# Kernel tuning notes

Hardware: AMD Instinct MI355X
Metric: run time of the kernel (lower is better)

## Reference

```python
import jax, jax.numpy as jnp
import numpy as np

N = 10000          # nodes
E_RAND = 320000    # random edges (avg degree 32)
F_IN = 512         # nfeat
HID = 256          # args.hid
HEADS = 8          # args.head
FH = HID // HEADS  # 32 per head
NCLASS = 40
TAU = 0.5
LAMDA = 0.5
K = 2


def setup_inputs() -> dict:
    key = jax.random.key(0)
    ks = jax.random.split(key, 16)
    # edge list: random edges + self-loops (so every dst segment is non-empty)
    src = jnp.concatenate([jax.random.randint(ks[0], (E_RAND,), 0, N), jnp.arange(N)])
    dst = jnp.concatenate([jax.random.randint(ks[1], (E_RAND,), 0, N), jnp.arange(N)])
    s = 0.05  # small init scale keeps exp() in attention/bind_loss stable
    return {
        "x": jax.random.normal(ks[2], (N, F_IN), jnp.float32),
        "src": src, "dst": dst,
        "W0": jax.random.normal(ks[3], (F_IN, HEADS, FH), jnp.float32) * s,
        "a0s": jax.random.normal(ks[4], (HEADS, FH), jnp.float32) * s,
        "a0d": jax.random.normal(ks[5], (HEADS, FH), jnp.float32) * s,
        "W1": jax.random.normal(ks[6], (HID, HEADS, FH), jnp.float32) * s,
        "a1s": jax.random.normal(ks[7], (HEADS, FH), jnp.float32) * s,
        "a1d": jax.random.normal(ks[8], (HEADS, FH), jnp.float32) * s,
        "W2": jax.random.normal(ks[9], (HID, HEADS, FH), jnp.float32) * s,
        "a2s": jax.random.normal(ks[10], (HEADS, FH), jnp.float32) * s,
        "a2d": jax.random.normal(ks[11], (HEADS, FH), jnp.float32) * s,
        "Wout": jax.random.normal(ks[12], (HID, HEADS, NCLASS), jnp.float32) * s,
        "aos": jax.random.normal(ks[13], (HEADS, NCLASS), jnp.float32) * s,
        "aod": jax.random.normal(ks[14], (HEADS, NCLASS), jnp.float32) * s,
    }


def _gat_layer(x, W, a_s, a_d, src, dst):
    """Sparse multi-head GAT layer: gather -> edge softmax -> scatter."""
    n = x.shape[0]
    h = jnp.einsum('nf,fhd->nhd', x, W)              # [N,H,Fh]
    es = jnp.sum(h * a_s, axis=-1)                    # [N,H]
    ed = jnp.sum(h * a_d, axis=-1)                    # [N,H]
    e = jax.nn.leaky_relu(es[src] + ed[dst], 0.2)     # [E,H]
    m = jax.ops.segment_max(e, dst, num_segments=n)   # per-dst max (stable softmax)
    w = jnp.exp(e - m[dst])
    z = jax.ops.segment_sum(w, dst, num_segments=n)
    alpha = w / z[dst]                                # [E,H]
    return jax.ops.segment_sum(alpha[:, :, None] * h[src], dst, num_segments=n)  # [N,H,Fh]


def _bind_loss(z):
    # z1 == z2 == z in the original call site: refl_sim == between_sim
    zn = z / jnp.maximum(jnp.linalg.norm(z, axis=1, keepdims=True), 1e-12)
    S = jnp.exp(jnp.matmul(zn, zn.T) / TAU)           # [N,N]
    d = jnp.diagonal(S)
    off = jnp.sum(S, axis=1) - d                      # masked (off-diagonal) row sum
    CT = -jnp.log(d / (off + off))                    # neg_c2.sum + neg_c3.sum
    return jnp.mean(CT)


def reference(x, src, dst, W0, a0s, a0d, W1, a1s, a1d, W2, a2s, a2d, Wout, aos, aod):
    layers = [(W0, a0s, a0d), (W1, a1s, a1d), (W2, a2s, a2d)]
    last = x
    loss = jnp.float32(0.0)
    for i, (W, as_, ad_) in enumerate(layers):
        cur = jax.nn.elu(_gat_layer(last, W, as_, ad_, src, dst))
        cur = cur.reshape(cur.shape[0], -1)           # concat heads -> [N, HID]
        if i > 0:
            beta = LAMDA / (i + 2)                    # MaskLayer(last, cur, lamda, i+2)
            cur = beta * last + (1.0 - beta) * cur
            if i % K == 0:
                loss = loss + _bind_loss(cur)
        last = cur
    out = _gat_layer(last, Wout, aos, aod, src, dst).mean(axis=1)  # avg heads -> [N,C]
    return (jax.nn.log_softmax(out, axis=1), loss)
```

## Files before the change

kernel.cpp:

```cpp
#include <hip/hip_runtime.h>
#include <hip/hip_bf16.h>
#include <math.h>

#define NN_F_IN   512
#define NN_HID    256
#define NN_HEADS  8
#define NN_FH     32
#define NN_NCLASS 40
#define TAU_F     0.5f
#define LAMDA_F   0.5f
#define ZN_SCALE  1.6986436f

typedef __attribute__((ext_vector_type(8))) short bf16x8;
typedef __attribute__((ext_vector_type(4))) float f32x4;

static __device__ __forceinline__ float lrelu02(float x) { return x >= 0.f ? x : 0.2f * x; }
static __device__ __forceinline__ float elu1(float x)    { return x > 0.f ? x : expm1f(x); }
static __device__ __forceinline__ float b2f(unsigned short u) {
    unsigned int x = ((unsigned int)u) << 16;
    return __uint_as_float(x);
}
static __device__ __forceinline__ unsigned short f2b(float f) {
    __hip_bfloat16 hb = __float2bfloat16(f);
    return *reinterpret_cast<unsigned short*>(&hb);
}

__global__ void prep_kernel(const float* __restrict__ x,
                            const float* __restrict__ W0, const float* __restrict__ W1,
                            const float* __restrict__ W2, const float* __restrict__ Wo,
                            unsigned short* __restrict__ Xb,
                            unsigned short* __restrict__ Wt0, unsigned short* __restrict__ Wt1,
                            unsigned short* __restrict__ Wt2, unsigned short* __restrict__ Wto,
                            int n4X) {
    int i = blockIdx.x * 256 + threadIdx.x;
    if (i < n4X) {
        float4 v = *(const float4*)(x + (size_t)i * 4);
        ushort4 o;
        o.x = f2b(v.x); o.y = f2b(v.y); o.z = f2b(v.z); o.w = f2b(v.w);
        *(ushort4*)(Xb + (size_t)i * 4) = o;
        return;
    }
    i -= n4X;
    if (i < 256 * 512) {
        int np = i >> 9, k = i & 511;
        Wt0[i] = f2b(W0[(size_t)k * 256 + np]);
        return;
    }
    i -= 256 * 512;
    if (i < 256 * 256) {
        int np = i >> 8, k = i & 255;
        Wt1[i] = f2b(W1[(size_t)k * 256 + np]);
        return;
    }
    i -= 256 * 256;
    if (i < 256 * 256) {
        int np = i >> 8, k = i & 255;
        Wt2[i] = f2b(W2[(size_t)k * 256 + np]);
        return;
    }
    i -= 256 * 256;
    if (i < 384 * 256) {
        int np = i >> 8, k = i & 255;
        Wto[i] = f2b(np < 320 ? Wo[(size_t)k * 320 + np] : 0.f);
    }
}

__global__ __launch_bounds__(256) void fc_attn_mfma(
    const unsigned short* __restrict__ A, const unsigned short* __restrict__ B,
    unsigned short* __restrict__ H, const float* __restrict__ As_,
    const float* __restrict__ Ad_, float* __restrict__ es, float* __restrict__ ed,
    int M, int K) {
    const int ldH = 256;
    int t = threadIdx.x, lane = t & 63, wid = t >> 6;
    int wrow = wid >> 1, wcol = wid & 1;
    int l15 = lane & 15, lg = lane >> 4;
    int mbase = blockIdx.y * 64 + wrow * 32;
    int nbase = blockIdx.x * 64 + wcol * 32;

    const unsigned short* Ap[2];
    const unsigned short* Bp[2];
#pragma unroll
    for (int m = 0; m < 2; ++m) {
        int rr = mbase + m * 16 + l15;
        if (rr > M - 1) rr = M - 1;
        Ap[m] = A + (size_t)rr * K + lg * 8;
        Bp[m] = B + (size_t)(nbase + m * 16 + l15) * K + lg * 8;
    }
    f32x4 acc[2][2];
#pragma unroll
    for (int m = 0; m < 2; ++m)
#pragma unroll
        for (int nn = 0; nn < 2; ++nn)
#pragma unroll
            for (int r = 0; r < 4; ++r) acc[m][nn][r] = 0.f;

    bf16x8 aP[2], bP[2], aQ[2], bQ[2];
#pragma unroll
    for (int m = 0; m < 2; ++m) {
        aP[m] = *(const bf16x8*)(Ap[m]);
        bP[m] = *(const bf16x8*)(Bp[m]);
    }
    int nhalf = K >> 6;
    int kk = 32;
    for (int it = 0; it < nhalf; ++it) {
#pragma unroll
        for (int m = 0; m < 2; ++m) {
            aQ[m] = *(const bf16x8*)(Ap[m] + kk);
            bQ[m] = *(const bf16x8*)(Bp[m] + kk);
        }
#pragma unroll
        for (int m = 0; m < 2; ++m)
#pragma unroll
            for (int nn = 0; nn < 2; ++nn)
                acc[m][nn] = __builtin_amdgcn_mfma_f32_16x16x32_bf16(aP[m], bP[nn], acc[m][nn], 0, 0, 0);
        if (it + 1 < nhalf) {
#pragma unroll
            for (int m = 0; m < 2; ++m) {
                aP[m] = *(const bf16x8*)(Ap[m] + kk + 32);
                bP[m] = *(const bf16x8*)(Bp[m] + kk + 32);
            }
        }
#pragma unroll
        for (int m = 0; m < 2; ++m)
#pragma unroll
            for (int nn = 0; nn < 2; ++nn)
                acc[m][nn] = __builtin_amdgcn_mfma_f32_16x16x32_bf16(aQ[m], bQ[nn], acc[m][nn], 0, 0, 0);
        kk += 64;
    }
#pragma unroll
    for (int m = 0; m < 2; ++m) {
#pragma unroll
        for (int nn = 0; nn < 2; ++nn) {
            int col = nbase + nn * 16 + l15;
#pragma unroll
            for (int r = 0; r < 4; ++r) {
                int row = mbase + m * 16 + lg * 4 + r;
                if (row < M) H[(size_t)row * ldH + col] = f2b(acc[m][nn][r]);
            }
        }
    }
    int hh = blockIdx.x * 2 + wcol;
    float a0 = As_[hh * 32 + l15], a1 = As_[hh * 32 + 16 + l15];
    float d0 = Ad_[hh * 32 + l15], d1 = Ad_[hh * 32 + 16 + l15];
#pragma unroll
    for (int m = 0; m < 2; ++m) {
#pragma unroll
        for (int r = 0; r < 4; ++r) {
            float ps = acc[m][0][r] * a0 + acc[m][1][r] * a1;
            float pd = acc[m][0][r] * d0 + acc[m][1][r] * d1;
            ps += __shfl_xor(ps, 1, 64); pd += __shfl_xor(pd, 1, 64);
            ps += __shfl_xor(ps, 2, 64); pd += __shfl_xor(pd, 2, 64);
            ps += __shfl_xor(ps, 4, 64); pd += __shfl_xor(pd, 4, 64);
            ps += __shfl_xor(ps, 8, 64); pd += __shfl_xor(pd, 8, 64);
            if (l15 == 0) {
                int row = mbase + m * 16 + lg * 4 + r;
                if (row < M) {
                    es[row * NN_HEADS + hh] = ps;
                    ed[row * NN_HEADS + hh] = pd;
                }
            }
        }
    }
}

__global__ __launch_bounds__(256) void fc_mfma(const unsigned short* __restrict__ A,
                                               const unsigned short* __restrict__ B,
                                               unsigned short* __restrict__ H,
                                               int M, int K, int ncols, int ldH) {
    int t = threadIdx.x, lane = t & 63, wid = t >> 6;
    int wrow = wid >> 1, wcol = wid & 1;
    int l15 = lane & 15, lg = lane >> 4;
    int mbase = blockIdx.y * 64 + wrow * 32;
    int nbase = blockIdx.x * 64 + wcol * 32;

    const unsigned short* Ap[2];
    const unsigned short* Bp[2];
#pragma unroll
    for (int m = 0; m < 2; ++m) {
        int rr = mbase + m * 16 + l15;
        if (rr > M - 1) rr = M - 1;
        Ap[m] = A + (size_t)rr * K + lg * 8;
        Bp[m] = B + (size_t)(nbase + m * 16 + l15) * K + lg * 8;
    }
    f32x4 acc[2][2];
#pragma unroll
    for (int m = 0; m < 2; ++m)
#pragma unroll
        for (int nn = 0; nn < 2; ++nn)
#pragma unroll
            for (int r = 0; r < 4; ++r) acc[m][nn][r] = 0.f;

    bf16x8 aP[2], bP[2], aQ[2], bQ[2];
#pragma unroll
    for (int m = 0; m < 2; ++m) {
        aP[m] = *(const bf16x8*)(Ap[m]);
        bP[m] = *(const bf16x8*)(Bp[m]);
    }
    int nhalf = K >> 6;
    int kk = 32;
    for (int it = 0; it < nhalf; ++it) {
#pragma unroll
        for (int m = 0; m < 2; ++m) {
            aQ[m] = *(const bf16x8*)(Ap[m] + kk);
            bQ[m] = *(const bf16x8*)(Bp[m] + kk);
        }
#pragma unroll
        for (int m = 0; m < 2; ++m)
#pragma unroll
            for (int nn = 0; nn < 2; ++nn)
                acc[m][nn] = __builtin_amdgcn_mfma_f32_16x16x32_bf16(aP[m], bP[nn], acc[m][nn], 0, 0, 0);
        if (it + 1 < nhalf) {
#pragma unroll
            for (int m = 0; m < 2; ++m) {
                aP[m] = *(const bf16x8*)(Ap[m] + kk + 32);
                bP[m] = *(const bf16x8*)(Bp[m] + kk + 32);
            }
        }
#pragma unroll
        for (int m = 0; m < 2; ++m)
#pragma unroll
            for (int nn = 0; nn < 2; ++nn)
                acc[m][nn] = __builtin_amdgcn_mfma_f32_16x16x32_bf16(aQ[m], bQ[nn], acc[m][nn], 0, 0, 0);
        kk += 64;
    }
#pragma unroll
    for (int m = 0; m < 2; ++m) {
#pragma unroll
        for (int nn = 0; nn < 2; ++nn) {
            int col = nbase + nn * 16 + l15;
            if (col >= ncols) continue;
#pragma unroll
            for (int r = 0; r < 4; ++r) {
                int row = mbase + m * 16 + lg * 4 + r;
                if (row < M) H[(size_t)row * ldH + col] = f2b(acc[m][nn][r]);
            }
        }
    }
}

__global__ void attn_kernel(const unsigned short* __restrict__ Hm, const float* __restrict__ As,
                            const float* __restrict__ Ad, float* __restrict__ es,
                            float* __restrict__ ed, int n, int df) {
    int idx = blockIdx.x * blockDim.x + threadIdx.x;
    if (idx >= n * NN_HEADS) return;
    int nn = idx / NN_HEADS, hh = idx - nn * NN_HEADS;
    const unsigned short* hp = Hm + (size_t)nn * NN_HEADS * df + hh * df;
    const float* ap = As + hh * df;
    const float* bp = Ad + hh * df;
    float s1 = 0.f, s2 = 0.f;
    for (int d = 0; d < df; d += 4) {
        ushort4 hv = *(const ushort4*)(hp + d);
        float4 av = *(const float4*)(ap + d);
        float4 bv = *(const float4*)(bp + d);
        float h0 = b2f(hv.x), h1 = b2f(hv.y), h2 = b2f(hv.z), h3 = b2f(hv.w);
        s1 += h0 * av.x + h1 * av.y + h2 * av.z + h3 * av.w;
        s2 += h0 * bv.x + h1 * bv.y + h2 * bv.z + h3 * bv.w;
    }
    es[idx] = s1;
    ed[idx] = s2;
}

__global__ __launch_bounds__(256) void edge_wz(
    const float* __restrict__ es, const float* __restrict__ ed,
    const int* __restrict__ csr_src, const int* __restrict__ row_start,
    float* __restrict__ wC, float* __restrict__ zinv, int n) {
    int lane = threadIdx.x & 63;
    int nn   = blockIdx.x * 4 + (threadIdx.x >> 6);
    if (nn >= n) return;
    int s0 = row_start[nn], s1 = row_start[nn + 1];
    int h    = lane & 7;
    int slot = lane >> 3;
    float edh = ed[nn * NN_HEADS + h];
    float z = 0.f;
    for (int e = s0 + slot; e < s1; e += 8) {
        int sv = csr_src[e];
        float w = __expf(lrelu02(es[sv * NN_HEADS + h] + edh));
        wC[(size_t)e * NN_HEADS + h] = w;
        z += w;
    }
    z += __shfl_xor(z, 8, 64);
    z += __shfl_xor(z, 16, 64);
    z += __shfl_xor(z, 32, 64);
    if (slot == 0) zinv[nn * NN_HEADS + h] = 1.f / z;
}

__global__ void count_kernel(const int* __restrict__ dst, int* __restrict__ counts, int E) {
    int e = blockIdx.x * blockDim.x + threadIdx.x;
    if (e < E) atomicAdd(&counts[dst[e]], 1);
}

__global__ void scan_kernel(const int* __restrict__ counts, int* __restrict__ row_start,
                            int* __restrict__ cursor, int n) {
    __shared__ int s[1024];
    int t  = threadIdx.x;
    int ch = (n + 1023) / 1024;
    int lo = t * ch;
    int sum = 0;
    for (int j = 0; j < ch; ++j) {
        int i = lo + j;
        if (i < n) sum += counts[i];
    }
    s[t] = sum;
    __syncthreads();
    for (int off = 1; off < 1024; off <<= 1) {
        int v = 0;
        if (t >= off) v = s[t - off];
        __syncthreads();
        s[t] += v;
        __syncthreads();
    }
    int run = (t == 0) ? 0 : s[t - 1];
    for (int j = 0; j < ch; ++j) {
        int i = lo + j;
        if (i < n) {
            row_start[i] = run;
            cursor[i] = run;
            run += counts[i];
        }
    }
    if (t == 1023) row_start[n] = s[1023];
}

__global__ void scatter_kernel(const int* __restrict__ src, const int* __restrict__ dst,
                               int* __restrict__ cursor, int* __restrict__ csr_src, int E) {
    int e = blockIdx.x * blockDim.x + threadIdx.x;
    if (e < E) {
        int d   = dst[e];
        int pos = atomicAdd(&cursor[d], 1);
        csr_src[pos] = src[e];
    }
}

__global__ __launch_bounds__(256) void gather_hidden(
    const unsigned short* __restrict__ Hm, const float* __restrict__ es,
    const float* __restrict__ ed, const int* __restrict__ csr_src,
    const int* __restrict__ row_start, const unsigned short* __restrict__ last,
    unsigned short* __restrict__ out, int n, float beta,
    unsigned short* __restrict__ znb, float* __restrict__ dvec) {
    int lane = threadIdx.x & 63;
    int nn   = blockIdx.x * 4 + (threadIdx.x >> 6);
    if (nn >= n) return;
    int s0 = row_start[nn], s1 = row_start[nn + 1];
    int h2 = lane >> 3;
    float edh = ed[nn * NN_HEADS + h2];

    float zacc = 0.f;
    float a0 = 0.f, a1 = 0.f, a2 = 0.f, a3 = 0.f;
    int fullEnd = s0 + ((s1 - s0) & ~15);
    int e = s0;
    for (; e < fullEnd; e += 16) {
        int idx[16];
        float q[16];
#pragma unroll
        for (int j = 0; j < 16; ++j) idx[j] = csr_src[e + j];
#pragma unroll
        for (int j = 0; j < 16; ++j) q[j] = es[idx[j] * NN_HEADS + h2];
        ushort4 r[16];
#pragma unroll
        for (int j = 0; j < 16; ++j) r[j] = *(const ushort4*)&Hm[(size_t)idx[j] * NN_HID + lane * 4];
#pragma unroll
        for (int j = 0; j < 16; ++j) {
            float w = __expf(lrelu02(q[j] + edh));
            zacc += w;
            a0 += w * b2f(r[j].x); a1 += w * b2f(r[j].y);
            a2 += w * b2f(r[j].z); a3 += w * b2f(r[j].w);
        }
    }
    if (e < s1) {
        int c = s1 - e;
        int idx[16];
        float q[16];
#pragma unroll
        for (int j = 0; j < 16; ++j) idx[j] = csr_src[(j < c) ? e + j : e];
#pragma unroll
        for (int j = 0; j < 16; ++j) q[j] = es[idx[j] * NN_HEADS + h2];
        ushort4 r[16];
#pragma unroll
        for (int j = 0; j < 16; ++j) r[j] = *(const ushort4*)&Hm[(size_t)idx[j] * NN_HID + lane * 4];
#pragma unroll
        for (int j = 0; j < 16; ++j) {
            if (j < c) {
                float w = __expf(lrelu02(q[j] + edh));
                zacc += w;
                a0 += w * b2f(r[j].x); a1 += w * b2f(r[j].y);
                a2 += w * b2f(r[j].z); a3 += w * b2f(r[j].w);
            }
        }
    }
    float zi = 1.f / zacc;
    float v0 = elu1(a0 * zi), v1 = elu1(a1 * zi), v2 = elu1(a2 * zi), v3 = elu1(a3 * zi);
    if (beta >= 0.f) {
        ushort4 lv = *(const ushort4*)&last[(size_t)nn * NN_HID + lane * 4];
        v0 = beta * b2f(lv.x) + (1.f - beta) * v0;
        v1 = beta * b2f(lv.y) + (1.f - beta) * v1;
        v2 = beta * b2f(lv.z) + (1.f - beta) * v2;
        v3 = beta * b2f(lv.w) + (1.f - beta) * v3;
    }
    ushort4 o;
    o.x = f2b(v0); o.y = f2b(v1); o.z = f2b(v2); o.w = f2b(v3);
    *(ushort4*)&out[(size_t)nn * NN_HID + lane * 4] = o;

    if (znb) {
        float ss = v0 * v0 + v1 * v1 + v2 * v2 + v3 * v3;
        ss += __shfl_xor(ss, 1, 64);
        ss += __shfl_xor(ss, 2, 64);
        ss += __shfl_xor(ss, 4, 64);
        ss += __shfl_xor(ss, 8, 64);
        ss += __shfl_xor(ss, 16, 64);
        ss += __shfl_xor(ss, 32, 64);
        float m = fmaxf(sqrtf(ss), 1e-12f);
        float sc = ZN_SCALE / m;
        ushort4 zo;
        zo.x = f2b(v0 * sc); zo.y = f2b(v1 * sc);
        zo.z = f2b(v2 * sc); zo.w = f2b(v3 * sc);
        *(ushort4*)&znb[(size_t)nn * NN_HID + lane * 4] = zo;
        if (lane == 0) dvec[nn] = __expf((ss / (m * m)) * (1.f / TAU_F));
    }
}

__global__ void gather_final(const unsigned short* __restrict__ Hm, const float* __restrict__ wC,
                             const float* __restrict__ zinv, const int* __restrict__ csr_src,
                             const int* __restrict__ row_start, float* __restrict__ dout, int n) {
    int nn = blockIdx.x;
    __shared__ float accs[NN_HEADS * NN_NCLASS];
    int t = threadIdx.x;
    int s0 = row_start[nn], s1 = row_start[nn + 1];
    int hh = t / NN_NCLASS;
    float acc = 0.f;
    const int LD = NN_HEADS * NN_NCLASS;
    int fullEnd = s0 + ((s1 - s0) & ~15);
    int e = s0;
    for (; e < fullEnd; e += 16) {
        int idx[16];
        float wv[16];
#pragma unroll
        for (int j = 0; j < 16; ++j) {
            idx[j] = csr_src[e + j];
            wv[j]  = wC[(size_t)(e + j) * NN_HEADS + hh];
        }
        float v[16];
#pragma unroll
        for (int j = 0; j < 16; ++j) v[j] = b2f(Hm[(size_t)idx[j] * LD + t]);
#pragma unroll
        for (int j = 0; j < 16; ++j) acc += wv[j] * v[j];
    }
    if (e < s1) {
        int c = s1 - e;
        int idx[16];
        float wv[16];
#pragma unroll
        for (int j = 0; j < 16; ++j) {
            int p = (j < c) ? e + j : e;
            idx[j] = csr_src[p];
            wv[j]  = wC[(size_t)p * NN_HEADS + hh];
        }
        float v[16];
#pragma unroll
        for (int j = 0; j < 16; ++j) v[j] = b2f(Hm[(size_t)idx[j] * LD + t]);
#pragma unroll
        for (int j = 0; j < 16; ++j) {
            if (j < c) acc += wv[j] * v[j];
        }
    }
    accs[t] = acc * zinv[nn * NN_HEADS + hh];
    __syncthreads();
    if (t < 64) {
        float v = -INFINITY;
        if (t < NN_NCLASS) {
            float sacc = 0.f;
#pragma unroll
            for (int h2 = 0; h2 < NN_HEADS; ++h2) sacc += accs[h2 * NN_NCLASS + t];
            v = sacc * (1.f / NN_HEADS);
        }
        float mx = v;
#pragma unroll
        for (int o = 1; o < 64; o <<= 1) mx = fmaxf(mx, __shfl_xor(mx, o, 64));
        float ex = (t < NN_NCLASS) ? expf(v - mx) : 0.f;
        float se = ex;
#pragma unroll
        for (int o = 1; o < 64; o <<= 1) se += __shfl_xor(se, o, 64);
        if (t < NN_NCLASS) dout[(size_t)nn * NN_NCLASS + t] = (v - mx) - logf(se);
    }
}

__global__ __launch_bounds__(256) void gram_mfma(const short* __restrict__ znb,
                                                 float* __restrict__ P2d, int n,
                                                 int T, int nwg, int Npad) {
    __shared__ short As[2][128 * 64];
    __shared__ short Bs[2][128 * 64];

    int b = blockIdx.x;
    int q = nwg >> 3, r8 = nwg & 7, xc = b & 7, oo = b >> 3;
    int sid = (xc < r8 ? xc * (q + 1) : r8 * (q + 1) + (xc - r8) * q) + oo;
    int bi = 0, rem = sid;
    while (rem >= T - bi) { rem -= T - bi; ++bi; }
    int bj = bi + rem;
    int i0 = bi * 128, j0 = bj * 128;

    int t    = threadIdx.x;
    int lane = t & 63;
    int wid  = t >> 6;
    int wrow = wid >> 1, wcol = wid & 1;
    int l15  = lane & 15, lg = lane >> 4;
    int srow = lane >> 3;
    int sch  = lane & 7;

    f32x4 acc[4][4];
#pragma unroll
    for (int m = 0; m < 4; ++m)
#pragma unroll
        for (int nn = 0; nn < 4; ++nn)
#pragma unroll
            for (int r = 0; r < 4; ++r) acc[m][nn][r] = 0.f;

    bf16x8 sa[2][4], sb[2][4];
#pragma unroll
    for (int sl = 0; sl < 2; ++sl)
#pragma unroll
        for (int s = 0; s < 4; ++s) {
            int row = wid * 32 + s * 8 + srow;
            int gch = sch ^ (row & 7);
            sa[sl][s] = *(const bf16x8*)(znb + (size_t)(i0 + row) * NN_HID + sl * 64 + gch * 8);
            sb[sl][s] = *(const bf16x8*)(znb + (size_t)(j0 + row) * NN_HID + sl * 64 + gch * 8);
        }

#pragma unroll
    for (int kt = 0; kt < 2; ++kt) {
#pragma unroll
        for (int sl = 0; sl < 2; ++sl)
#pragma unroll
            for (int s = 0; s < 4; ++s) {
                int row = wid * 32 + s * 8 + srow;
                *(bf16x8*)(&As[sl][row * 64 + sch * 8]) = sa[sl][s];
                *(bf16x8*)(&Bs[sl][row * 64 + sch * 8]) = sb[sl][s];
            }
        __syncthreads();
        if (kt == 0) {
#pragma unroll
            for (int sl = 0; sl < 2; ++sl)
#pragma unroll
                for (int s = 0; s < 4; ++s) {
                    int row = wid * 32 + s * 8 + srow;
                    int gch = sch ^ (row & 7);
                    sa[sl][s] = *(const bf16x8*)(znb + (size_t)(i0 + row) * NN_HID + 128 + sl * 64 + gch * 8);
                    sb[sl][s] = *(const bf16x8*)(znb + (size_t)(j0 + row) * NN_HID + 128 + sl * 64 + gch * 8);
                }
        }
#pragma unroll
        for (int sl = 0; sl < 2; ++sl) {
#pragma unroll
            for (int ks = 0; ks < 2; ++ks) {
                bf16x8 av[4], bv[4];
#pragma unroll
                for (int m = 0; m < 4; ++m) {
                    int Ra = wrow * 64 + m * 16 + l15;
                    int Rb = wcol * 64 + m * 16 + l15;
                    int ca = (ks * 4 + lg) ^ (Ra & 7);
                    int cb = (ks * 4 + lg) ^ (Rb & 7);
                    av[m] = *(const bf16x8*)(&As[sl][Ra * 64 + ca * 8]);
                    bv[m] = *(const bf16x8*)(&Bs[sl][Rb * 64 + cb * 8]);
                }
#pragma unroll
                for (int m = 0; m < 4; ++m)
#pragma unroll
                    for (int nn = 0; nn < 4; ++nn)
                        acc[m][nn] = __builtin_amdgcn_mfma_f32_16x16x32_bf16(av[m], bv[nn], acc[m][nn], 0, 0, 0);
            }
        }
        if (kt == 0) __syncthreads();
    }

    int i0w = i0 + wrow * 64;
    int j0w = j0 + wcol * 64;
    bool diag = (bj == bi);
    if (bj == T - 1) {
#pragma unroll
        for (int m = 0; m < 4; ++m)
#pragma unroll
            for (int nn = 0; nn < 4; ++nn) {
                int gj = j0w + nn * 16 + l15;
                bool jok = gj < n;
#pragma unroll
                for (int r = 0; r < 4; ++r) {
                    int gi = i0w + m * 16 + lg * 4 + r;
                    acc[m][nn][r] = (jok && gi < n) ? __builtin_exp2f(acc[m][nn][r]) : 0.f;
                }
            }
    } else {
#pragma unroll
        for (int m = 0; m < 4; ++m)
#pragma unroll
            for (int nn = 0; nn < 4; ++nn)
#pragma unroll
                for (int r = 0; r < 4; ++r)
                    acc[m][nn][r] = __builtin_exp2f(acc[m][nn][r]);
    }
    float* rowslot = P2d + (size_t)(2 * bj + wcol) * Npad;
#pragma unroll
    for (int m = 0; m < 4; ++m) {
#pragma unroll
        for (int r = 0; r < 4; ++r) {
            float v = acc[m][0][r] + acc[m][1][r] + acc[m][2][r] + acc[m][3][r];
            v += __shfl_xor(v, 1, 64);
            v += __shfl_xor(v, 2, 64);
            v += __shfl_xor(v, 4, 64);
            v += __shfl_xor(v, 8, 64);
            if (l15 == 0) {
                int gi = i0w + m * 16 + lg * 4 + r;
                if (gi < n) rowslot[gi] = v;
            }
        }
    }
    if (!diag) {
        float* colslot = P2d + (size_t)(2 * bi + wrow) * Npad;
#pragma unroll
        for (int nn = 0; nn < 4; ++nn) {
            float v = 0.f;
#pragma unroll
            for (int m = 0; m < 4; ++m)
#pragma unroll
                for (int r = 0; r < 4; ++r) v += acc[m][nn][r];
            v += __shfl_xor(v, 16, 64);
            v += __shfl_xor(v, 32, 64);
            if (lg == 0) {
                int gj = j0w + nn * 16 + l15;
                if (gj < n) colslot[gj] = v;
            }
        }
    }
}

__global__ void fold_kernel(const float* __restrict__ P2d, float* __restrict__ R,
                            int n, int slots, int Npad) {
    int i = blockIdx.x * 256 + threadIdx.x;
    if (i >= n) return;
    const float* p = P2d + i;
    float s0 = 0.f, s1 = 0.f, s2 = 0.f, s3 = 0.f;
    int sl = 0;
    for (; sl + 4 <= slots; sl += 4) {
        s0 += p[(size_t)(sl + 0) * Npad];
        s1 += p[(size_t)(sl + 1) * Npad];
        s2 += p[(size_t)(sl + 2) * Npad];
        s3 += p[(size_t)(sl + 3) * Npad];
    }
    for (; sl < slots; ++sl) s0 += p[(size_t)sl * Npad];
    R[i] = (s0 + s1) + (s2 + s3);
}

__global__ void loss_kernel(const float* __restrict__ R, const float* __restrict__ dvec,
                            float* __restrict__ out_loss, int n) {
    __shared__ float s[1024];
    int t = threadIdx.x;
    float sum = 0.f;
    for (int i = t; i < n; i += 1024) {
        float d   = dvec[i];
        float off = R[i] - d;
        sum += -logf(d / (off + off));
    }
    s[t] = sum;
    __syncthreads();
    for (int o = 512; o > 0; o >>= 1) {
        if (t < o) s[t] += s[t + o];
        __syncthreads();
    }
    if (t == 0) *out_loss = s[0] / n;
}

extern "C" void kernel_launch(void* const* d_in, const int* in_sizes, int n_in,
                              void* d_out, int out_size, void* d_ws, size_t ws_size,
                              hipStream_t stream) {
    const float* x   = (const float*)d_in[0];
    const int*   src = (const int*)d_in[1];
    const int*   dst = (const int*)d_in[2];
    const float* W0  = (const float*)d_in[3];
    const float* a0s = (const float*)d_in[4];
    const float* a0d = (const float*)d_in[5];
    const float* W1  = (const float*)d_in[6];
    const float* a1s = (const float*)d_in[7];
    const float* a1d = (const float*)d_in[8];
    const float* W2  = (const float*)d_in[9];
    const float* a2s = (const float*)d_in[10];
    const float* a2d = (const float*)d_in[11];
    const float* Wout= (const float*)d_in[12];
    const float* aos = (const float*)d_in[13];
    const float* aod = (const float*)d_in[14];

    int N = in_sizes[0] / NN_F_IN;
    int E = in_sizes[1];
    int Npad = ((N + 127) / 128) * 128;
    int T = Npad / 128;
    int nwg = T * (T + 1) / 2;
    float* out = (float*)d_out;

    char*  ws  = (char*)d_ws;
    size_t off = 0;
    auto alloc = [&](size_t bytes) -> void* {
        void* p = ws + off;
        off += bytes;
        off = (off + 255) & ~(size_t)255;
        return p;
    };
    unsigned short* Hb = (unsigned short*)alloc((size_t)N * 320 * 2);
    unsigned short* znb = (unsigned short*)alloc((size_t)Npad * NN_HID * 2);
    unsigned short* Bl = (unsigned short*)alloc((size_t)N * NN_HID * 2);
    unsigned short* Bc = (unsigned short*)alloc((size_t)N * NN_HID * 2);
    size_t xbBytes = (size_t)N * NN_F_IN * 2;
    size_t p2Bytes = (size_t)2 * T * Npad * 4;
    void* XbP2d = alloc(xbBytes > p2Bytes ? xbBytes : p2Bytes);
    unsigned short* Xb  = (unsigned short*)XbP2d;
    float*          P2d = (float*)XbP2d;
    unsigned short* Wt0 = (unsigned short*)alloc((size_t)256 * 512 * 2);
    unsigned short* Wt1 = (unsigned short*)alloc((size_t)256 * 256 * 2);
    unsigned short* Wt2 = (unsigned short*)alloc((size_t)256 * 256 * 2);
    unsigned short* Wto = (unsigned short*)alloc((size_t)384 * 256 * 2);
    float* es     = (float*)alloc((size_t)N * NN_HEADS * 4);
    float* ed     = (float*)alloc((size_t)N * NN_HEADS * 4);
    float* wC     = (float*)alloc((size_t)E * NN_HEADS * 4);
    float* zinvA  = (float*)alloc((size_t)N * NN_HEADS * 4);
    float* Rrow   = (float*)alloc((size_t)N * 4);
    float* dvec   = (float*)alloc((size_t)N * 4);
    int*   counts = (int*)alloc((size_t)N * 4);
    int*   rs     = (int*)alloc((size_t)(N + 1) * 4);
    int*   cursor = (int*)alloc((size_t)N * 4);
    int*   csr    = (int*)alloc((size_t)E * 4);

    hipMemsetAsync(counts, 0, (size_t)N * 4, stream);
    if (Npad > N)
        hipMemsetAsync(znb + (size_t)N * NN_HID, 0, (size_t)(Npad - N) * NN_HID * 2, stream);
    count_kernel<<<(E + 255) / 256, 256, 0, stream>>>(dst, counts, E);
    scan_kernel<<<1, 1024, 0, stream>>>(counts, rs, cursor, N);
    scatter_kernel<<<(E + 255) / 256, 256, 0, stream>>>(src, dst, cursor, csr, E);

    int n4X = N * NN_F_IN / 4;
    int prepTotal = n4X + 256 * 512 + 256 * 256 + 256 * 256 + 384 * 256;
    prep_kernel<<<(prepTotal + 255) / 256, 256, 0, stream>>>(
        x, W0, W1, W2, Wout, Xb, Wt0, Wt1, Wt2, Wto, n4X);

    int atGrid = (N * NN_HEADS + 255) / 256;
    int ghGrid = (N + 3) / 4;
    int mT64 = (N + 63) / 64;

    fc_attn_mfma<<<dim3(4, mT64), 256, 0, stream>>>(Xb, Wt0, Hb, a0s, a0d, es, ed, N, 512);
    gather_hidden<<<ghGrid, 256, 0, stream>>>(Hb, es, ed, csr, rs, nullptr, Bl, N, -1.f,
                                              nullptr, nullptr);

    fc_attn_mfma<<<dim3(4, mT64), 256, 0, stream>>>(Bl, Wt1, Hb, a1s, a1d, es, ed, N, 256);
    gather_hidden<<<ghGrid, 256, 0, stream>>>(Hb, es, ed, csr, rs, Bl, Bc, N, LAMDA_F / 3.f,
                                              nullptr, nullptr);

    fc_attn_mfma<<<dim3(4, mT64), 256, 0, stream>>>(Bc, Wt2, Hb, a2s, a2d, es, ed, N, 256);
    gather_hidden<<<ghGrid, 256, 0, stream>>>(Hb, es, ed, csr, rs, Bc, Bl, N, LAMDA_F / 4.f,
                                              znb, dvec);

    gram_mfma<<<nwg, 256, 0, stream>>>((const short*)znb, P2d, N, T, nwg, Npad);
    fold_kernel<<<(N + 255) / 256, 256, 0, stream>>>(P2d, Rrow, N, 2 * T, Npad);
    loss_kernel<<<1, 1024, 0, stream>>>(Rrow, dvec, out + (size_t)N * NN_NCLASS, N);

    fc_mfma<<<dim3(5, mT64), 256, 0, stream>>>(Bl, Wto, Hb, N, 256, 320, 320);
    attn_kernel<<<atGrid, 256, 0, stream>>>(Hb, aos, aod, es, ed, N, NN_NCLASS);
    edge_wz<<<ghGrid, 256, 0, stream>>>(es, ed, csr, rs, wC, zinvA, N);
    gather_final<<<N, NN_HEADS * NN_NCLASS, 0, stream>>>(Hb, wC, zinvA, csr, rs, out, N);
}
```

Measured before the change: 375.5 us.

## Merge output FC GEMM into gram kernel launch and halve gather unroll

The output-layer FC GEMM is folded into the gram kernel as extra leading blocks. The FC tiles then run alongside the gram tiles in one launch instead of after them, and the attention and edge-weight kernels are moved ahead of the fold and loss kernels. Separately, the gather loops in gather_hidden and gather_final are unrolled by 8 instead of 16, trading memory-level parallelism for lower register pressure and a smaller tail. The FC blocks now share the gram kernel's large LDS allocation even though they don't use it, which may cap co-residency for those blocks.

```diff
diff --git a/kernel.cpp b/kernel.cpp
--- a/kernel.cpp
+++ b/kernel.cpp
@@ -158,81 +158,6 @@
                     es[row * NN_HEADS + hh] = ps;
                     ed[row * NN_HEADS + hh] = pd;
                 }
-            }
-        }
-    }
-}
-
-__global__ __launch_bounds__(256) void fc_mfma(const unsigned short* __restrict__ A,
-                                               const unsigned short* __restrict__ B,
-                                               unsigned short* __restrict__ H,
-                                               int M, int K, int ncols, int ldH) {
-    int t = threadIdx.x, lane = t & 63, wid = t >> 6;
-    int wrow = wid >> 1, wcol = wid & 1;
-    int l15 = lane & 15, lg = lane >> 4;
-    int mbase = blockIdx.y * 64 + wrow * 32;
-    int nbase = blockIdx.x * 64 + wcol * 32;
-
-    const unsigned short* Ap[2];
-    const unsigned short* Bp[2];
-#pragma unroll
-    for (int m = 0; m < 2; ++m) {
-        int rr = mbase + m * 16 + l15;
-        if (rr > M - 1) rr = M - 1;
-        Ap[m] = A + (size_t)rr * K + lg * 8;
-        Bp[m] = B + (size_t)(nbase + m * 16 + l15) * K + lg * 8;
-    }
-    f32x4 acc[2][2];
-#pragma unroll
-    for (int m = 0; m < 2; ++m)
-#pragma unroll
-        for (int nn = 0; nn < 2; ++nn)
-#pragma unroll
-            for (int r = 0; r < 4; ++r) acc[m][nn][r] = 0.f;
-
-    bf16x8 aP[2], bP[2], aQ[2], bQ[2];
-#pragma unroll
-    for (int m = 0; m < 2; ++m) {
-        aP[m] = *(const bf16x8*)(Ap[m]);
-        bP[m] = *(const bf16x8*)(Bp[m]);
-    }
-    int nhalf = K >> 6;
-    int kk = 32;
-    for (int it = 0; it < nhalf; ++it) {
-#pragma unroll
-        for (int m = 0; m < 2; ++m) {
-            aQ[m] = *(const bf16x8*)(Ap[m] + kk);
-            bQ[m] = *(const bf16x8*)(Bp[m] + kk);
-        }
-#pragma unroll
-        for (int m = 0; m < 2; ++m)
-#pragma unroll
-            for (int nn = 0; nn < 2; ++nn)
-                acc[m][nn] = __builtin_amdgcn_mfma_f32_16x16x32_bf16(aP[m], bP[nn], acc[m][nn], 0, 0, 0);
-        if (it + 1 < nhalf) {
-#pragma unroll
-            for (int m = 0; m < 2; ++m) {
-                aP[m] = *(const bf16x8*)(Ap[m] + kk + 32);
-                bP[m] = *(const bf16x8*)(Bp[m] + kk + 32);
-            }
-        }
-#pragma unroll
-        for (int m = 0; m < 2; ++m)
-#pragma unroll
-            for (int nn = 0; nn < 2; ++nn)
-                acc[m][nn] = __builtin_amdgcn_mfma_f32_16x16x32_bf16(aQ[m], bQ[nn], acc[m][nn], 0, 0, 0);
-        kk += 64;
-    }
-#pragma unroll
-    for (int m = 0; m < 2; ++m) {
-#pragma unroll
-        for (int nn = 0; nn < 2; ++nn) {
-            int col = nbase + nn * 16 + l15;
-            if (col >= ncols) continue;
-#pragma unroll
-            for (int r = 0; r < 4; ++r) {
-                int row = mbase + m * 16 + lg * 4 + r;
-                if (row < M) H[(size_t)row * ldH + col] = f2b(acc[m][nn][r]);
             }
         }
     }
@@ -346,20 +271,20 @@
 
     float zacc = 0.f;
     float a0 = 0.f, a1 = 0.f, a2 = 0.f, a3 = 0.f;
-    int fullEnd = s0 + ((s1 - s0) & ~15);
+    int fullEnd = s0 + ((s1 - s0) & ~7);
     int e = s0;
-    for (; e < fullEnd; e += 16) {
-        int idx[16];
-        float q[16];
-#pragma unroll
-        for (int j = 0; j < 16; ++j) idx[j] = csr_src[e + j];
-#pragma unroll
-        for (int j = 0; j < 16; ++j) q[j] = es[idx[j] * NN_HEADS + h2];
-        ushort4 r[16];
-#pragma unroll
-        for (int j = 0; j < 16; ++j) r[j] = *(const ushort4*)&Hm[(size_t)idx[j] * NN_HID + lane * 4];
-#pragma unroll
-        for (int j = 0; j < 16; ++j) {
+    for (; e < fullEnd; e += 8) {
+        int idx[8];
+        float q[8];
+#pragma unroll
+        for (int j = 0; j < 8; ++j) idx[j] = csr_src[e + j];
+#pragma unroll
+        for (int j = 0; j < 8; ++j) q[j] = es[idx[j] * NN_HEADS + h2];
+        ushort4 r[8];
+#pragma unroll
+        for (int j = 0; j < 8; ++j) r[j] = *(const ushort4*)&Hm[(size_t)idx[j] * NN_HID + lane * 4];
+#pragma unroll
+        for (int j = 0; j < 8; ++j) {
             float w = __expf(lrelu02(q[j] + edh));
             zacc += w;
             a0 += w * b2f(r[j].x); a1 += w * b2f(r[j].y);
@@ -368,17 +293,17 @@
     }
     if (e < s1) {
         int c = s1 - e;
-        int idx[16];
-        float q[16];
-#pragma unroll
-        for (int j = 0; j < 16; ++j) idx[j] = csr_src[(j < c) ? e + j : e];
-#pragma unroll
-        for (int j = 0; j < 16; ++j) q[j] = es[idx[j] * NN_HEADS + h2];
-        ushort4 r[16];
-#pragma unroll
-        for (int j = 0; j < 16; ++j) r[j] = *(const ushort4*)&Hm[(size_t)idx[j] * NN_HID + lane * 4];
-#pragma unroll
-        for (int j = 0; j < 16; ++j) {
+        int idx[8];
+        float q[8];
+#pragma unroll
+        for (int j = 0; j < 8; ++j) idx[j] = csr_src[(j < c) ? e + j : e];
+#pragma unroll
+        for (int j = 0; j < 8; ++j) q[j] = es[idx[j] * NN_HEADS + h2];
+        ushort4 r[8];
+#pragma unroll
+        for (int j = 0; j < 8; ++j) r[j] = *(const ushort4*)&Hm[(size_t)idx[j] * NN_HID + lane * 4];
+#pragma unroll
+        for (int j = 0; j < 8; ++j) {
             if (j < c) {
                 float w = __expf(lrelu02(q[j] + edh));
                 zacc += w;
@@ -428,37 +353,37 @@
     int hh = t / NN_NCLASS;
     float acc = 0.f;
     const int LD = NN_HEADS * NN_NCLASS;
-    int fullEnd = s0 + ((s1 - s0) & ~15);
+    int fullEnd = s0 + ((s1 - s0) & ~7);
     int e = s0;
-    for (; e < fullEnd; e += 16) {
-        int idx[16];
-        float wv[16];
-#pragma unroll
-        for (int j = 0; j < 16; ++j) {
+    for (; e < fullEnd; e += 8) {
+        int idx[8];
+        float wv[8];
+#pragma unroll
+        for (int j = 0; j < 8; ++j) {
             idx[j] = csr_src[e + j];
             wv[j]  = wC[(size_t)(e + j) * NN_HEADS + hh];
         }
-        float v[16];
-#pragma unroll
-        for (int j = 0; j < 16; ++j) v[j] = b2f(Hm[(size_t)idx[j] * LD + t]);
-#pragma unroll
-        for (int j = 0; j < 16; ++j) acc += wv[j] * v[j];
+        float v[8];
+#pragma unroll
+        for (int j = 0; j < 8; ++j) v[j] = b2f(Hm[(size_t)idx[j] * LD + t]);
+#pragma unroll
+        for (int j = 0; j < 8; ++j) acc += wv[j] * v[j];
     }
     if (e < s1) {
         int c = s1 - e;
-        int idx[16];
-        float wv[16];
-#pragma unroll
-        for (int j = 0; j < 16; ++j) {
+        int idx[8];
+        float wv[8];
+#pragma unroll
+        for (int j = 0; j < 8; ++j) {
             int p = (j < c) ? e + j : e;
             idx[j] = csr_src[p];
             wv[j]  = wC[(size_t)p * NN_HEADS + hh];
         }
-        float v[16];
-#pragma unroll
-        for (int j = 0; j < 16; ++j) v[j] = b2f(Hm[(size_t)idx[j] * LD + t]);
-#pragma unroll
-        for (int j = 0; j < 16; ++j) {
+        float v[8];
+#pragma unroll
+        for (int j = 0; j < 8; ++j) v[j] = b2f(Hm[(size_t)idx[j] * LD + t]);
+#pragma unroll
+        for (int j = 0; j < 8; ++j) {
             if (j < c) acc += wv[j] * v[j];
         }
     }
@@ -483,13 +408,94 @@
     }
 }
 
-__global__ __launch_bounds__(256) void gram_mfma(const short* __restrict__ znb,
-                                                 float* __restrict__ P2d, int n,
-                                                 int T, int nwg, int Npad) {
+__global__ __launch_bounds__(256) void gram_fc_mfma(
+    const short* __restrict__ znb, float* __restrict__ P2d, int n,
+    int T, int nwg, int Npad,
+    const unsigned short* __restrict__ A, const unsigned short* __restrict__ Bw,
+    unsigned short* __restrict__ H, int M, int nfc, int fcX) {
     __shared__ short As[2][128 * 64];
     __shared__ short Bs[2][128 * 64];
 
-    int b = blockIdx.x;
+    int t    = threadIdx.x;
+    int lane = t & 63;
+    int wid  = t >> 6;
+    int l15  = lane & 15, lg = lane >> 4;
+
+    if (blockIdx.x < nfc) {
+        const int K = 256, ncols = 320, ldH = 320;
+        int idx = blockIdx.x;
+        int bx = idx % fcX, by = idx / fcX;
+        int wrow = wid >> 1, wcol = wid & 1;
+        int mbase = by * 64 + wrow * 32;
+        int nbase = bx * 64 + wcol * 32;
+
+        const unsigned short* Ap[2];
+        const unsigned short* Bp[2];
+#pragma unroll
+        for (int m = 0; m < 2; ++m) {
+            int rr = mbase + m * 16 + l15;
+            if (rr > M - 1) rr = M - 1;
+            Ap[m] = A + (size_t)rr * K + lg * 8;
+            Bp[m] = Bw + (size_t)(nbase + m * 16 + l15) * K + lg * 8;
+        }
+        f32x4 acc[2][2];
+#pragma unroll
+        for (int m = 0; m < 2; ++m)
+#pragma unroll
+            for (int nn = 0; nn < 2; ++nn)
+#pragma unroll
+                for (int r = 0; r < 4; ++r) acc[m][nn][r] = 0.f;
+
+        bf16x8 aP[2], bP[2], aQ[2], bQ[2];
+#pragma unroll
+        for (int m = 0; m < 2; ++m) {
+            aP[m] = *(const bf16x8*)(Ap[m]);
+            bP[m] = *(const bf16x8*)(Bp[m]);
+        }
+        int kk = 32;
+#pragma unroll
+        for (int it = 0; it < 4; ++it) {
+#pragma unroll
+            for (int m = 0; m < 2; ++m) {
+                aQ[m] = *(const bf16x8*)(Ap[m] + kk);
+                bQ[m] = *(const bf16x8*)(Bp[m] + kk);
+            }
+#pragma unroll
+            for (int m = 0; m < 2; ++m)
+#pragma unroll
+                for (int nn = 0; nn < 2; ++nn)
+                    acc[m][nn] = __builtin_amdgcn_mfma_f32_16x16x32_bf16(aP[m], bP[nn], acc[m][nn], 0, 0, 0);
+            if (it < 3) {
+#pragma unroll
+                for (int m = 0; m < 2; ++m) {
+                    aP[m] = *(const bf16x8*)(Ap[m] + kk + 32);
+                    bP[m] = *(const bf16x8*)(Bp[m] + kk + 32);
+                }
+            }
+#pragma unroll
+            for (int m = 0; m < 2; ++m)
+#pragma unroll
+                for (int nn = 0; nn < 2; ++nn)
+                    acc[m][nn] = __builtin_amdgcn_mfma_f32_16x16x32_bf16(aQ[m], bQ[nn], acc[m][nn], 0, 0, 0);
+            kk += 64;
+        }
+#pragma unroll
+        for (int m = 0; m < 2; ++m) {
+#pragma unroll
+            for (int nn = 0; nn < 2; ++nn) {
+                int col = nbase + nn * 16 + l15;
+                if (col >= ncols) continue;
+#pragma unroll
+                for (int r = 0; r < 4; ++r) {
+                    int row = mbase + m * 16 + lg * 4 + r;
+                    if (row < M) H[(size_t)row * ldH + col] = f2b(acc[m][nn][r]);
+                }
+            }
+        }
+        return;
+    }
+
+    int b = blockIdx.x - nfc;
     int q = nwg >> 3, r8 = nwg & 7, xc = b & 7, oo = b >> 3;
     int sid = (xc < r8 ? xc * (q + 1) : r8 * (q + 1) + (xc - r8) * q) + oo;
     int bi = 0, rem = sid;
@@ -497,11 +503,7 @@
     int bj = bi + rem;
     int i0 = bi * 128, j0 = bj * 128;
 
-    int t    = threadIdx.x;
-    int lane = t & 63;
-    int wid  = t >> 6;
     int wrow = wid >> 1, wcol = wid & 1;
-    int l15  = lane & 15, lg = lane >> 4;
     int srow = lane >> 3;
     int sch  = lane & 7;
 
@@ -752,12 +754,14 @@
     gather_hidden<<<ghGrid, 256, 0, stream>>>(Hb, es, ed, csr, rs, Bc, Bl, N, LAMDA_F / 4.f,
                                               znb, dvec);
 
-    gram_mfma<<<nwg, 256, 0, stream>>>((const short*)znb, P2d, N, T, nwg, Npad);
+    int fcX = 5;
+    int nfc = fcX * mT64;
+    gram_fc_mfma<<<nfc + nwg, 256, 0, stream>>>((const short*)znb, P2d, N, T, nwg, Npad,
+                                                Bl, Wto, Hb, N, nfc, fcX);
+
+    attn_kernel<<<atGrid, 256, 0, stream>>>(Hb, aos, aod, es, ed, N, NN_NCLASS);
+    edge_wz<<<ghGrid, 256, 0, stream>>>(es, ed, csr, rs, wC, zinvA, N);
     fold_kernel<<<(N + 255) / 256, 256, 0, stream>>>(P2d, Rrow, N, 2 * T, Npad);
     loss_kernel<<<1, 1024, 0, stream>>>(Rrow, dvec, out + (size_t)N * NN_NCLASS, N);
-
-    fc_mfma<<<dim3(5, mT64), 256, 0, stream>>>(Bl, Wto, Hb, N, 256, 320, 320);
-    attn_kernel<<<atGrid, 256, 0, stream>>>(Hb, aos, aod, es, ed, N, NN_NCLASS);
-    edge_wz<<<ghGrid, 256, 0, stream>>>(es, ed, csr, rs, wC, zinvA, N);
     gather_final<<<N, NN_HEADS * NN_NCLASS, 0, stream>>>(Hb, wC, zinvA, csr, rs, out, N);
 }
```

After: 352.0 us. 6.3% less time.
